# Kernel tuning notes

Hardware: AMD Instinct MI355X
Metric: run time of the kernel (lower is better)

The kernel has to match this reference:

```python
import jax, jax.numpy as jnp
import numpy as np

T, D, H, E, K = 8192, 512, 1024, 16, 2  # tokens, d_model, d_hidden, num_expert, top_k


def setup_inputs() -> dict:
    key = jax.random.key(0)
    ks = jax.random.split(key, 4)
    return {
        "x": jax.random.normal(ks[0], (T, D), jnp.float32),
        "Wg": jax.random.normal(ks[1], (D, E), jnp.float32) * (D ** -0.5),
        "bg": jnp.zeros((E,), jnp.float32),
        "W1": jax.random.normal(ks[2], (E, D, H), jnp.float32) * (D ** -0.5),
        "b1": jnp.zeros((E, H), jnp.float32),
        "W2": jax.random.normal(ks[3], (E, H, D), jnp.float32) * (H ** -0.5),
        "b2": jnp.zeros((E, D), jnp.float32),
    }


def _moe(x, Wg, bg, W1, b1, W2, b2):
    # NaiveGate: linear -> top-k -> softmax over the k selected logits
    logits = x @ Wg + bg                              # [T, E]
    top_val, top_idx = jax.lax.top_k(logits, K)       # [T, K]
    score = jax.nn.softmax(top_val, axis=-1)          # [T, K]
    # Dispatch + per-expert MLP + combine. Mathematically identical to the
    # scatter/grouped-GEMM/gather: for each expert, the per-token combine
    # weight is the gate score if the token routed there, else 0.
    out = jnp.zeros_like(x)
    for e in range(E):  # fixed small loop over structurally distinct experts
        h = jax.nn.gelu(x @ W1[e] + b1[e], approximate=False)  # [T, H]
        y = h @ W2[e] + b2[e]                                   # [T, D]
        w_e = jnp.sum(jnp.where(top_idx == e, score, 0.0), axis=-1)  # [T]
        out = out + w_e[:, None] * y
    return out


def reference(x, Wg, bg, W1, b1, W2, b2):
    return _moe(x, Wg, bg, W1, b1, W2, b2)
```

## Files before the change

kernel.cpp:

```cpp
#include <hip/hip_runtime.h>
#include <hip/hip_bf16.h>
#include <math.h>

#define TT 8192
#define DD 512
#define HH 1024
#define EE 16
#define NSLOT 18432
#define MAXTILES 144
#define BM 128
#define RETRYCAP 1024

typedef __attribute__((ext_vector_type(8))) short bf16x8;
typedef __attribute__((ext_vector_type(8))) unsigned short u16x8;
typedef __attribute__((ext_vector_type(4))) float f32x4;

__device__ __forceinline__ unsigned short f2bf(float f) {
  union { float f; unsigned u; } v; v.f = f;
  unsigned r = v.u + 0x7fffu + ((v.u >> 16) & 1u);
  return (unsigned short)(r >> 16);
}

__device__ __forceinline__ float bf2f(unsigned short u) {
  union { unsigned u; float f; } v; v.u = ((unsigned)u) << 16;
  return v.f;
}

__device__ __forceinline__ void gload16(const void* g, void* l) {
  __builtin_amdgcn_global_load_lds(
      (const __attribute__((address_space(1))) unsigned int*)g,
      (__attribute__((address_space(3))) unsigned int*)l, 16, 0, 0);
}

__device__ __forceinline__ float gelu_f(float v) {
  float s = fabsf(v) * 0.70710678118654752f;
  float t = 1.0f / (1.0f + 0.3275911f * s);
  float poly = t * (0.254829592f +
              t * (-0.284496736f +
              t * (1.421413741f +
              t * (-1.453152027f +
              t * 1.061405429f))));
  float erfa = 1.0f - poly * __expf(-s * s);
  float erfv = (v >= 0.f) ? erfa : -erfa;
  return 0.5f * v * (1.0f + erfv);
}

__device__ __forceinline__ int tile_decode(const int* __restrict__ counts,
                                           int mt, int* e_out, int* row0_out) {
  int off = 0, rem = mt;
#pragma unroll
  for (int q = 0; q < EE; q++) {
    int tl = (counts[q] + BM - 1) / BM;
    if (rem < tl) { *e_out = q; *row0_out = off + rem * BM; return 1; }
    rem -= tl;
    off += tl * BM;
  }
  return 0;
}

__global__ __launch_bounds__(256) void prep_kernel(
    const float* __restrict__ W1, const float* __restrict__ W2,
    unsigned short* __restrict__ w1t, unsigned short* __restrict__ w2t,
    const float* __restrict__ x, const float* __restrict__ Wg,
    const float* __restrict__ bg, unsigned short* __restrict__ xb,
    int* __restrict__ gate_e, float* __restrict__ gate_w,
    int* __restrict__ counts, int* __restrict__ nretry,
    int* __restrict__ retry) {
  __shared__ union { unsigned short t[64][68]; int cnt[EE]; } sm;
  int bid = blockIdx.x;
  int tid = threadIdx.x;
  if (bid < 128) {
    int lane = tid & 63;
    int wave = tid >> 6;
    int tok0 = bid * 64 + wave * 16;
    if (tid < EE) sm.cnt[tid] = 0;
    __syncthreads();
    int e = lane & 15;
    int kb = (lane >> 4) * 8;
    bf16x8 bfrag[16];
#pragma unroll
    for (int ks = 0; ks < 16; ks++) {
      int kbase = ks * 32 + kb;
#pragma unroll
      for (int j = 0; j < 8; j++)
        bfrag[ks][j] = (short)f2bf(Wg[(kbase + j) * EE + e]);
    }
    float bge = bg[e];
    f32x4 acc = {0.f, 0.f, 0.f, 0.f};
    const float* xrow = x + (size_t)(tok0 + (lane & 15)) * DD + kb;
    unsigned short* xbrow = xb + (size_t)(tok0 + (lane & 15)) * DD + kb;
#pragma unroll 4
    for (int ks = 0; ks < 16; ks++) {
      int k0 = ks * 32;
      float4 v0 = *(const float4*)(xrow + k0);
      float4 v1 = *(const float4*)(xrow + k0 + 4);
      u16x8 w0;
      w0[0] = f2bf(v0.x); w0[1] = f2bf(v0.y); w0[2] = f2bf(v0.z); w0[3] = f2bf(v0.w);
      w0[4] = f2bf(v1.x); w0[5] = f2bf(v1.y); w0[6] = f2bf(v1.z); w0[7] = f2bf(v1.w);
      *(u16x8*)(xbrow + k0) = w0;
      union { u16x8 u; bf16x8 b; } cv; cv.u = w0;
      acc = __builtin_amdgcn_mfma_f32_16x16x32_bf16(cv.b, bfrag[ks], acc, 0, 0, 0);
    }
#pragma unroll
    for (int r = 0; r < 4; r++) {
      float lf = acc[r] + bge;
      float v1 = -1e30f, v2 = -1e30f, v3 = -1e30f;
      int i1 = 0, i2 = 0;
#pragma unroll
      for (int q = 0; q < EE; q++) {
        float v = __shfl(lf, (lane & 48) | q);
        if (v > v1) { v3 = v2; v2 = v1; i2 = i1; v1 = v; i1 = q; }
        else if (v > v2) { v3 = v2; v2 = v; i2 = q; }
        else if (v > v3) { v3 = v; }
      }
      if ((lane & 15) == 0) {
        int t2 = tok0 + ((lane >> 4) << 2) + r;
        float p = expf(v2 - v1);
        float s = 1.0f / (1.0f + p);
        gate_e[t2 * 2] = i1;
        gate_e[t2 * 2 + 1] = i2;
        gate_w[t2 * 2] = s;
        gate_w[t2 * 2 + 1] = p * s;
        atomicAdd(&sm.cnt[i1], 1);
        atomicAdd(&sm.cnt[i2], 1);
        if (v2 - v3 < 0.02f) {
          int pos = atomicAdd(nretry, 1);
          if (pos < RETRYCAP) retry[pos] = t2;
        }
      }
    }
    __syncthreads();
    if (tid < EE) atomicAdd(&counts[tid], sm.cnt[tid]);
    return;
  }
  const float* src;
  unsigned short* dst;
  int R, C, c0, r0;
  int b = bid - 128;
  if (b < 2048) {
    int cx = b & 15, ry = (b >> 4) & 7, mat = b >> 7;
    src = W1 + (size_t)mat * DD * HH; dst = w1t + (size_t)mat * DD * HH;
    R = DD; C = HH; c0 = cx * 64; r0 = ry * 64;
  } else {
    b -= 2048;
    int cx = b & 7, ry = (b >> 3) & 15, mat = b >> 7;
    src = W2 + (size_t)mat * DD * HH; dst = w2t + (size_t)mat * DD * HH;
    R = HH; C = DD; c0 = cx * 64; r0 = ry * 64;
  }
#pragma unroll
  for (int p = 0; p < 4; p++) {
    int r = tid >> 2;
    int c4 = (tid & 3) + p * 4;
    float4 v = *(const float4*)(src + (size_t)(r0 + r) * C + c0 + c4 * 4);
    sm.t[c4 * 4 + 0][r] = f2bf(v.x);
    sm.t[c4 * 4 + 1][r] = f2bf(v.y);
    sm.t[c4 * 4 + 2][r] = f2bf(v.z);
    sm.t[c4 * 4 + 3][r] = f2bf(v.w);
  }
  __syncthreads();
#pragma unroll
  for (int p = 0; p < 4; p++) {
    int oc = (tid >> 4) + p * 16;
    int ch = tid & 15;
    ushort4 v = *(ushort4*)(&sm.t[oc][ch * 4]);
    *(ushort4*)(dst + (size_t)(c0 + oc) * R + r0 + ch * 4) = v;
  }
}

__global__ __launch_bounds__(256) void gatefix_kernel(
    const float* __restrict__ x, const float* __restrict__ Wg,
    const float* __restrict__ bg, const int* __restrict__ nretry,
    const int* __restrict__ retry, int* __restrict__ gate_e,
    float* __restrict__ gate_w, int* __restrict__ counts) {
  __shared__ float lg[16][17];
  __shared__ int toks[16];
  int tid = threadIdx.x;
  int sl = tid >> 4, e = tid & 15;
  int s = blockIdx.x * 16 + sl;
  int n = *nretry; if (n > RETRYCAP) n = RETRYCAP;
  int active = (s < n);
  int tok = 0;
  if (active) tok = retry[s];
  if (active) {
    const float* xr = x + (size_t)tok * DD;
    double a0 = 0.0, a1 = 0.0, a2 = 0.0, a3 = 0.0;
    for (int i = 0; i < DD / 4; i++) {
      a0 += (double)xr[i * 4 + 0] * (double)Wg[(i * 4 + 0) * EE + e];
      a1 += (double)xr[i * 4 + 1] * (double)Wg[(i * 4 + 1) * EE + e];
      a2 += (double)xr[i * 4 + 2] * (double)Wg[(i * 4 + 2) * EE + e];
      a3 += (double)xr[i * 4 + 3] * (double)Wg[(i * 4 + 3) * EE + e];
    }
    double acc = (a0 + a1) + (a2 + a3);
    lg[sl][e] = (float)(acc + (double)bg[e]);
    toks[sl] = tok;
  }
  __syncthreads();
  if (active && e == 0) {
    float v1 = -1e30f, v2 = -1e30f;
    int i1 = 0, i2 = 0;
#pragma unroll
    for (int q = 0; q < EE; q++) {
      float v = lg[sl][q];
      if (v > v1) { v2 = v1; i2 = i1; v1 = v; i1 = q; }
      else if (v > v2) { v2 = v; i2 = q; }
    }
    int t2 = toks[sl];
    int o1 = gate_e[t2 * 2], o2 = gate_e[t2 * 2 + 1];
    float p = expf(v2 - v1);
    float sc = 1.0f / (1.0f + p);
    gate_e[t2 * 2] = i1;
    gate_e[t2 * 2 + 1] = i2;
    gate_w[t2 * 2] = sc;
    gate_w[t2 * 2 + 1] = p * sc;
    if (o1 != i1 || o2 != i2) {
      atomicSub(&counts[o1], 1);
      atomicSub(&counts[o2], 1);
      atomicAdd(&counts[i1], 1);
      atomicAdd(&counts[i2], 1);
    }
  }
}

__global__ __launch_bounds__(256) void scatter_kernel(
    const int* __restrict__ gate_e, const float* __restrict__ gate_w,
    const int* __restrict__ counts, int* __restrict__ fill,
    int* __restrict__ slot_token, float* __restrict__ slot_w,
    int* __restrict__ slot_of) {
  __shared__ int lcnt[EE];
  __shared__ int lbase[EE];
  __shared__ int offs_s[EE];
  int tid = threadIdx.x;
  int t = blockIdx.x * 256 + tid;
  if (tid < EE) lcnt[tid] = 0;
  if (tid == 0) {
    int off = 0;
    for (int q = 0; q < EE; q++) {
      offs_s[q] = off;
      off += ((counts[q] + BM - 1) / BM) * BM;
    }
  }
  __syncthreads();
  if (blockIdx.x == 0) {
#pragma unroll
    for (int q = 0; q < EE; q++) {
      int cnt = counts[q];
      int lim = ((cnt + BM - 1) / BM) * BM;
      for (int p = cnt + tid; p < lim; p += 256)
        slot_token[offs_s[q] + p] = -1;
    }
  }
  int e0 = gate_e[t * 2], e1 = gate_e[t * 2 + 1];
  int p0 = atomicAdd(&lcnt[e0], 1);
  int p1 = atomicAdd(&lcnt[e1], 1);
  __syncthreads();
  if (tid < EE) lbase[tid] = atomicAdd(&fill[tid], lcnt[tid]);
  __syncthreads();
  int s0 = offs_s[e0] + lbase[e0] + p0;
  int s1 = offs_s[e1] + lbase[e1] + p1;
  slot_token[s0] = t;
  slot_w[s0] = gate_w[t * 2];
  slot_of[t * 2] = s0;
  slot_token[s1] = t;
  slot_w[s1] = gate_w[t * 2 + 1];
  slot_of[t * 2 + 1] = s1;
}

__global__ __launch_bounds__(256) void gemm1_kernel(
    const unsigned short* __restrict__ xb, const unsigned short* __restrict__ w1t,
    const float* __restrict__ b1, const int* __restrict__ slot_token,
    const int* __restrict__ counts, unsigned short* __restrict__ hb) {
  int e, row0;
  if (!tile_decode(counts, blockIdx.y, &e, &row0)) return;
  int n0 = blockIdx.x * 128;
  __shared__ unsigned short As[3][128][32];
  __shared__ unsigned short Bs[3][128][32];
  int tid = threadIdx.x;
  int lane = tid & 63;
  int wave = tid >> 6;
  int wm = wave >> 1, wn = wave & 1;
  int ra = tid >> 2, c = tid & 3;
  int tok_a = slot_token[row0 + ra]; if (tok_a < 0) tok_a = 0;
  int tok_b = slot_token[row0 + ra + 64]; if (tok_b < 0) tok_b = 0;
  const unsigned short* wbase = w1t + ((size_t)e * HH * DD);
  const unsigned short* gA0 = xb + (size_t)tok_a * DD + c * 8;
  const unsigned short* gA1 = xb + (size_t)tok_b * DD + c * 8;
  const unsigned short* gB0 = wbase + (size_t)(n0 + ra) * DD + c * 8;
  const unsigned short* gB1 = wbase + (size_t)(n0 + ra + 64) * DD + c * 8;
  f32x4 acc[4][4];
#pragma unroll
  for (int m = 0; m < 4; m++)
#pragma unroll
    for (int n = 0; n < 4; n++) {
      f32x4 z = {0.f, 0.f, 0.f, 0.f};
      acc[m][n] = z;
    }
  const int NK = DD / 32;
#pragma unroll
  for (int p = 0; p < 2; p++) {
    int kj = p * 32;
    gload16(gA0 + kj, &As[p][ra][c * 8]);
    gload16(gA1 + kj, &As[p][ra + 64][c * 8]);
    gload16(gB0 + kj, &Bs[p][ra][c * 8]);
    gload16(gB1 + kj, &Bs[p][ra + 64][c * 8]);
  }
  for (int kk = 0; kk < NK; kk++) {
    int cur = kk % 3;
    if (kk + 2 < NK) {
      int k2 = (kk + 2) * 32;
      int nx = (kk + 2) % 3;
      gload16(gA0 + k2, &As[nx][ra][c * 8]);
      gload16(gA1 + k2, &As[nx][ra + 64][c * 8]);
      gload16(gB0 + k2, &Bs[nx][ra][c * 8]);
      gload16(gB1 + k2, &Bs[nx][ra + 64][c * 8]);
      asm volatile("s_waitcnt vmcnt(8)" ::: "memory");
    } else if (kk + 1 < NK) {
      asm volatile("s_waitcnt vmcnt(4)" ::: "memory");
    } else {
      asm volatile("s_waitcnt vmcnt(0)" ::: "memory");
    }
    __builtin_amdgcn_s_barrier();
    bf16x8 a[4], b[4];
#pragma unroll
    for (int m = 0; m < 4; m++)
      a[m] = *(const bf16x8*)(&As[cur][wm * 64 + m * 16 + (lane & 15)][(lane >> 4) * 8]);
#pragma unroll
    for (int n = 0; n < 4; n++)
      b[n] = *(const bf16x8*)(&Bs[cur][wn * 64 + n * 16 + (lane & 15)][(lane >> 4) * 8]);
#pragma unroll
    for (int m = 0; m < 4; m++)
#pragma unroll
      for (int n = 0; n < 4; n++)
        acc[m][n] = __builtin_amdgcn_mfma_f32_16x16x32_bf16(a[m], b[n], acc[m][n], 0, 0, 0);
    asm volatile("" ::: "memory");
    __builtin_amdgcn_s_barrier();
  }
  const float* b1e = b1 + (size_t)e * HH;
#pragma unroll
  for (int m = 0; m < 4; m++) {
#pragma unroll
    for (int r = 0; r < 4; r++) {
      int slot = row0 + wm * 64 + m * 16 + ((lane >> 4) << 2) + r;
      unsigned short* hrow = hb + (size_t)slot * HH;
#pragma unroll
      for (int n = 0; n < 4; n++) {
        int hc = n0 + wn * 64 + n * 16 + (lane & 15);
        float v = acc[m][n][r] + b1e[hc];
        hrow[hc] = f2bf(gelu_f(v));
      }
    }
  }
}

template <int USE_Y>
__global__ __launch_bounds__(256) void gemm2_kernel(
    const unsigned short* __restrict__ hb, const unsigned short* __restrict__ w2t,
    const float* __restrict__ b2, const int* __restrict__ slot_token,
    const float* __restrict__ slot_w, const int* __restrict__ counts,
    unsigned short* __restrict__ yw, float* __restrict__ out) {
  int e, row0;
  if (!tile_decode(counts, blockIdx.y, &e, &row0)) return;
  int n0 = blockIdx.x * 128;
  __shared__ unsigned short As[3][128][32];
  __shared__ unsigned short Bs[3][128][32];
  int tid = threadIdx.x;
  int lane = tid & 63;
  int wave = tid >> 6;
  int wm = wave >> 1, wn = wave & 1;
  int ra = tid >> 2, c = tid & 3;
  const unsigned short* wbase = w2t + ((size_t)e * DD * HH);
  const unsigned short* gA0 = hb + (size_t)(row0 + ra) * HH + c * 8;
  const unsigned short* gA1 = hb + (size_t)(row0 + ra + 64) * HH + c * 8;
  const unsigned short* gB0 = wbase + (size_t)(n0 + ra) * HH + c * 8;
  const unsigned short* gB1 = wbase + (size_t)(n0 + ra + 64) * HH + c * 8;
  f32x4 acc[4][4];
#pragma unroll
  for (int m = 0; m < 4; m++)
#pragma unroll
    for (int n = 0; n < 4; n++) {
      f32x4 z = {0.f, 0.f, 0.f, 0.f};
      acc[m][n] = z;
    }
  const int NK = HH / 32;
#pragma unroll
  for (int p = 0; p < 2; p++) {
    int kj = p * 32;
    gload16(gA0 + kj, &As[p][ra][c * 8]);
    gload16(gA1 + kj, &As[p][ra + 64][c * 8]);
    gload16(gB0 + kj, &Bs[p][ra][c * 8]);
    gload16(gB1 + kj, &Bs[p][ra + 64][c * 8]);
  }
  for (int kk = 0; kk < NK; kk++) {
    int cur = kk % 3;
    if (kk + 2 < NK) {
      int k2 = (kk + 2) * 32;
      int nx = (kk + 2) % 3;
      gload16(gA0 + k2, &As[nx][ra][c * 8]);
      gload16(gA1 + k2, &As[nx][ra + 64][c * 8]);
      gload16(gB0 + k2, &Bs[nx][ra][c * 8]);
      gload16(gB1 + k2, &Bs[nx][ra + 64][c * 8]);
      asm volatile("s_waitcnt vmcnt(8)" ::: "memory");
    } else if (kk + 1 < NK) {
      asm volatile("s_waitcnt vmcnt(4)" ::: "memory");
    } else {
      asm volatile("s_waitcnt vmcnt(0)" ::: "memory");
    }
    __builtin_amdgcn_s_barrier();
    bf16x8 a[4], b[4];
#pragma unroll
    for (int m = 0; m < 4; m++)
      a[m] = *(const bf16x8*)(&As[cur][wm * 64 + m * 16 + (lane & 15)][(lane >> 4) * 8]);
#pragma unroll
    for (int n = 0; n < 4; n++)
      b[n] = *(const bf16x8*)(&Bs[cur][wn * 64 + n * 16 + (lane & 15)][(lane >> 4) * 8]);
#pragma unroll
    for (int m = 0; m < 4; m++)
#pragma unroll
      for (int n = 0; n < 4; n++)
        acc[m][n] = __builtin_amdgcn_mfma_f32_16x16x32_bf16(a[m], b[n], acc[m][n], 0, 0, 0);
    asm volatile("" ::: "memory");
    __builtin_amdgcn_s_barrier();
  }
  const float* b2e = b2 + (size_t)e * DD;
#pragma unroll
  for (int m = 0; m < 4; m++) {
#pragma unroll
    for (int r = 0; r < 4; r++) {
      int slot = row0 + wm * 64 + m * 16 + ((lane >> 4) << 2) + r;
      if (USE_Y) {
        float w = slot_w[slot];
        unsigned short* yrow = yw + (size_t)slot * DD;
#pragma unroll
        for (int n = 0; n < 4; n++) {
          int dc = n0 + wn * 64 + n * 16 + (lane & 15);
          yrow[dc] = f2bf(w * (acc[m][n][r] + b2e[dc]));
        }
      } else {
        int tok = slot_token[slot];
        if (tok >= 0) {
          float w = slot_w[slot];
          float* orow = out + (size_t)tok * DD;
#pragma unroll
          for (int n = 0; n < 4; n++) {
            int dc = n0 + wn * 64 + n * 16 + (lane & 15);
            float v = acc[m][n][r] + b2e[dc];
            atomicAdd(&orow[dc], w * v);
          }
        }
      }
    }
  }
}

__global__ __launch_bounds__(256) void combine_kernel(
    const unsigned short* __restrict__ yw, const int* __restrict__ slot_of,
    float* __restrict__ out) {
  int gid = blockIdx.x * 256 + threadIdx.x;
  int t = gid >> 6;
  int d0 = (gid & 63) * 8;
  int s1 = slot_of[t * 2], s2 = slot_of[t * 2 + 1];
  const ushort4* p1 = (const ushort4*)(yw + (size_t)s1 * DD + d0);
  const ushort4* p2 = (const ushort4*)(yw + (size_t)s2 * DD + d0);
  ushort4 a0 = p1[0], a1 = p1[1];
  ushort4 b0 = p2[0], b1 = p2[1];
  float4 o0, o1;
  o0.x = bf2f(a0.x) + bf2f(b0.x);
  o0.y = bf2f(a0.y) + bf2f(b0.y);
  o0.z = bf2f(a0.z) + bf2f(b0.z);
  o0.w = bf2f(a0.w) + bf2f(b0.w);
  o1.x = bf2f(a1.x) + bf2f(b1.x);
  o1.y = bf2f(a1.y) + bf2f(b1.y);
  o1.z = bf2f(a1.z) + bf2f(b1.z);
  o1.w = bf2f(a1.w) + bf2f(b1.w);
  float* orow = out + (size_t)t * DD + d0;
  ((float4*)orow)[0] = o0;
  ((float4*)orow)[1] = o1;
}

extern "C" void kernel_launch(void* const* d_in, const int* in_sizes, int n_in,
                              void* d_out, int out_size, void* d_ws, size_t ws_size,
                              hipStream_t stream) {
  const float* x  = (const float*)d_in[0];
  const float* Wg = (const float*)d_in[1];
  const float* bg = (const float*)d_in[2];
  const float* W1 = (const float*)d_in[3];
  const float* b1 = (const float*)d_in[4];
  const float* W2 = (const float*)d_in[5];
  const float* b2 = (const float*)d_in[6];
  float* out = (float*)d_out;

  uint8_t* w = (uint8_t*)d_ws;
  size_t o = 0;
  unsigned short* xb  = (unsigned short*)(w + o); o += (size_t)TT * DD * 2;
  unsigned short* w1t = (unsigned short*)(w + o); o += (size_t)EE * DD * HH * 2;
  unsigned short* w2t = (unsigned short*)(w + o); o += (size_t)EE * DD * HH * 2;
  unsigned short* hb  = (unsigned short*)(w + o); o += (size_t)NSLOT * HH * 2;
  int*   slot_token = (int*)(w + o);   o += (size_t)NSLOT * 4;
  float* slot_w     = (float*)(w + o); o += (size_t)NSLOT * 4;
  int*   slot_of    = (int*)(w + o);   o += (size_t)TT * 2 * 4;
  int*   gate_e     = (int*)(w + o);   o += (size_t)TT * 2 * 4;
  float* gate_w     = (float*)(w + o); o += (size_t)TT * 2 * 4;
  int*   counts     = (int*)(w + o);   o += 64;
  int*   nretry     = (int*)(w + o);   o += 64;
  int*   fill       = (int*)(w + o);   o += 64;
  int*   retry      = (int*)(w + o);   o += RETRYCAP * 4;
  unsigned short* yw = (unsigned short*)(w + o);
  size_t need_y = o + (size_t)NSLOT * DD * 2;
  int use_y = (ws_size >= need_y);

  hipMemsetAsync(counts, 0, 192, stream);
  if (!use_y) {
    hipMemsetAsync(slot_token, 0xFF, (size_t)NSLOT * 4, stream);
    hipMemsetAsync(d_out, 0, (size_t)TT * DD * 4, stream);
  }

  prep_kernel<<<128 + 4096, 256, 0, stream>>>(
      W1, W2, w1t, w2t, x, Wg, bg, xb, gate_e, gate_w, counts, nretry, retry);
  gatefix_kernel<<<RETRYCAP / 16, 256, 0, stream>>>(x, Wg, bg, nretry, retry,
                                                    gate_e, gate_w, counts);
  scatter_kernel<<<TT / 256, 256, 0, stream>>>(gate_e, gate_w, counts, fill,
                                               slot_token, slot_w, slot_of);
  {
    dim3 g(HH / 128, MAXTILES);
    gemm1_kernel<<<g, 256, 0, stream>>>(xb, w1t, b1, slot_token, counts, hb);
  }
  {
    dim3 g(DD / 128, MAXTILES);
    if (use_y)
      gemm2_kernel<1><<<g, 256, 0, stream>>>(hb, w2t, b2, slot_token, slot_w,
                                             counts, yw, out);
    else
      gemm2_kernel<0><<<g, 256, 0, stream>>>(hb, w2t, b2, slot_token, slot_w,
                                             counts, yw, out);
  }
  if (use_y) {
    combine_kernel<<<TT * (DD / 8) / 256, 256, 0, stream>>>(yw, slot_of, out);
  }
}
```

Measured before the change: 167.9 us.

## Widen GEMM tiles to 128x256 with 512 threads and double buffering

Both expert GEMMs now use 8 waves per block and a 128x256 output tile, halving the grid's N dimension. The shared-memory pipeline drops from triple to double buffering with one K-step of prefetch. Wider tiles let each A tile be reused across twice as many columns, cutting redundant global loads of gathered token rows. The costs are a shallower prefetch that may expose more memory latency, and fewer blocks in flight (grids of 4x144 and 2x144 on a 256-CU part), which risks poor load balance.

```diff
diff --git a/kernel.cpp b/kernel.cpp
--- a/kernel.cpp
+++ b/kernel.cpp
@@ -265,27 +265,25 @@
   slot_of[t * 2 + 1] = s1;
 }
 
-__global__ __launch_bounds__(256) void gemm1_kernel(
+__global__ __launch_bounds__(512) void gemm1_kernel(
     const unsigned short* __restrict__ xb, const unsigned short* __restrict__ w1t,
     const float* __restrict__ b1, const int* __restrict__ slot_token,
     const int* __restrict__ counts, unsigned short* __restrict__ hb) {
   int e, row0;
   if (!tile_decode(counts, blockIdx.y, &e, &row0)) return;
-  int n0 = blockIdx.x * 128;
-  __shared__ unsigned short As[3][128][32];
-  __shared__ unsigned short Bs[3][128][32];
+  int n0 = blockIdx.x * 256;
+  __shared__ unsigned short As[2][128][32];
+  __shared__ unsigned short Bs[2][256][32];
   int tid = threadIdx.x;
   int lane = tid & 63;
   int wave = tid >> 6;
-  int wm = wave >> 1, wn = wave & 1;
+  int wm = wave >> 2, wn = wave & 3;
   int ra = tid >> 2, c = tid & 3;
   int tok_a = slot_token[row0 + ra]; if (tok_a < 0) tok_a = 0;
-  int tok_b = slot_token[row0 + ra + 64]; if (tok_b < 0) tok_b = 0;
   const unsigned short* wbase = w1t + ((size_t)e * HH * DD);
-  const unsigned short* gA0 = xb + (size_t)tok_a * DD + c * 8;
-  const unsigned short* gA1 = xb + (size_t)tok_b * DD + c * 8;
+  const unsigned short* gA  = xb + (size_t)tok_a * DD + c * 8;
   const unsigned short* gB0 = wbase + (size_t)(n0 + ra) * DD + c * 8;
-  const unsigned short* gB1 = wbase + (size_t)(n0 + ra + 64) * DD + c * 8;
+  const unsigned short* gB1 = wbase + (size_t)(n0 + ra + 128) * DD + c * 8;
   f32x4 acc[4][4];
 #pragma unroll
   for (int m = 0; m < 4; m++)
@@ -295,26 +293,18 @@
       acc[m][n] = z;
     }
   const int NK = DD / 32;
-#pragma unroll
-  for (int p = 0; p < 2; p++) {
-    int kj = p * 32;
-    gload16(gA0 + kj, &As[p][ra][c * 8]);
-    gload16(gA1 + kj, &As[p][ra + 64][c * 8]);
-    gload16(gB0 + kj, &Bs[p][ra][c * 8]);
-    gload16(gB1 + kj, &Bs[p][ra + 64][c * 8]);
-  }
+  gload16(gA, &As[0][ra][c * 8]);
+  gload16(gB0, &Bs[0][ra][c * 8]);
+  gload16(gB1, &Bs[0][ra + 128][c * 8]);
   for (int kk = 0; kk < NK; kk++) {
-    int cur = kk % 3;
-    if (kk + 2 < NK) {
-      int k2 = (kk + 2) * 32;
-      int nx = (kk + 2) % 3;
-      gload16(gA0 + k2, &As[nx][ra][c * 8]);
-      gload16(gA1 + k2, &As[nx][ra + 64][c * 8]);
-      gload16(gB0 + k2, &Bs[nx][ra][c * 8]);
-      gload16(gB1 + k2, &Bs[nx][ra + 64][c * 8]);
-      asm volatile("s_waitcnt vmcnt(8)" ::: "memory");
-    } else if (kk + 1 < NK) {
-      asm volatile("s_waitcnt vmcnt(4)" ::: "memory");
+    int cur = kk & 1;
+    if (kk + 1 < NK) {
+      int k1 = (kk + 1) * 32;
+      int nx = cur ^ 1;
+      gload16(gA + k1, &As[nx][ra][c * 8]);
+      gload16(gB0 + k1, &Bs[nx][ra][c * 8]);
+      gload16(gB1 + k1, &Bs[nx][ra + 128][c * 8]);
+      asm volatile("s_waitcnt vmcnt(3)" ::: "memory");
     } else {
       asm volatile("s_waitcnt vmcnt(0)" ::: "memory");
     }
@@ -352,26 +342,25 @@
 }
 
 template <int USE_Y>
-__global__ __launch_bounds__(256) void gemm2_kernel(
+__global__ __launch_bounds__(512) void gemm2_kernel(
     const unsigned short* __restrict__ hb, const unsigned short* __restrict__ w2t,
     const float* __restrict__ b2, const int* __restrict__ slot_token,
     const float* __restrict__ slot_w, const int* __restrict__ counts,
     unsigned short* __restrict__ yw, float* __restrict__ out) {
   int e, row0;
   if (!tile_decode(counts, blockIdx.y, &e, &row0)) return;
-  int n0 = blockIdx.x * 128;
-  __shared__ unsigned short As[3][128][32];
-  __shared__ unsigned short Bs[3][128][32];
+  int n0 = blockIdx.x * 256;
+  __shared__ unsigned short As[2][128][32];
+  __shared__ unsigned short Bs[2][256][32];
   int tid = threadIdx.x;
   int lane = tid & 63;
   int wave = tid >> 6;
-  int wm = wave >> 1, wn = wave & 1;
+  int wm = wave >> 2, wn = wave & 3;
   int ra = tid >> 2, c = tid & 3;
   const unsigned short* wbase = w2t + ((size_t)e * DD * HH);
-  const unsigned short* gA0 = hb + (size_t)(row0 + ra) * HH + c * 8;
-  const unsigned short* gA1 = hb + (size_t)(row0 + ra + 64) * HH + c * 8;
+  const unsigned short* gA  = hb + (size_t)(row0 + ra) * HH + c * 8;
   const unsigned short* gB0 = wbase + (size_t)(n0 + ra) * HH + c * 8;
-  const unsigned short* gB1 = wbase + (size_t)(n0 + ra + 64) * HH + c * 8;
+  const unsigned short* gB1 = wbase + (size_t)(n0 + ra + 128) * HH + c * 8;
   f32x4 acc[4][4];
 #pragma unroll
   for (int m = 0; m < 4; m++)
@@ -381,26 +370,18 @@
       acc[m][n] = z;
     }
   const int NK = HH / 32;
-#pragma unroll
-  for (int p = 0; p < 2; p++) {
-    int kj = p * 32;
-    gload16(gA0 + kj, &As[p][ra][c * 8]);
-    gload16(gA1 + kj, &As[p][ra + 64][c * 8]);
-    gload16(gB0 + kj, &Bs[p][ra][c * 8]);
-    gload16(gB1 + kj, &Bs[p][ra + 64][c * 8]);
-  }
+  gload16(gA, &As[0][ra][c * 8]);
+  gload16(gB0, &Bs[0][ra][c * 8]);
+  gload16(gB1, &Bs[0][ra + 128][c * 8]);
   for (int kk = 0; kk < NK; kk++) {
-    int cur = kk % 3;
-    if (kk + 2 < NK) {
-      int k2 = (kk + 2) * 32;
-      int nx = (kk + 2) % 3;
-      gload16(gA0 + k2, &As[nx][ra][c * 8]);
-      gload16(gA1 + k2, &As[nx][ra + 64][c * 8]);
-      gload16(gB0 + k2, &Bs[nx][ra][c * 8]);
-      gload16(gB1 + k2, &Bs[nx][ra + 64][c * 8]);
-      asm volatile("s_waitcnt vmcnt(8)" ::: "memory");
-    } else if (kk + 1 < NK) {
-      asm volatile("s_waitcnt vmcnt(4)" ::: "memory");
+    int cur = kk & 1;
+    if (kk + 1 < NK) {
+      int k1 = (kk + 1) * 32;
+      int nx = cur ^ 1;
+      gload16(gA + k1, &As[nx][ra][c * 8]);
+      gload16(gB0 + k1, &Bs[nx][ra][c * 8]);
+      gload16(gB1 + k1, &Bs[nx][ra + 128][c * 8]);
+      asm volatile("s_waitcnt vmcnt(3)" ::: "memory");
     } else {
       asm volatile("s_waitcnt vmcnt(0)" ::: "memory");
     }
@@ -520,16 +501,16 @@
   scatter_kernel<<<TT / 256, 256, 0, stream>>>(gate_e, gate_w, counts, fill,
                                                slot_token, slot_w, slot_of);
   {
-    dim3 g(HH / 128, MAXTILES);
-    gemm1_kernel<<<g, 256, 0, stream>>>(xb, w1t, b1, slot_token, counts, hb);
+    dim3 g(HH / 256, MAXTILES);
+    gemm1_kernel<<<g, 512, 0, stream>>>(xb, w1t, b1, slot_token, counts, hb);
   }
   {
-    dim3 g(DD / 128, MAXTILES);
+    dim3 g(DD / 256, MAXTILES);
     if (use_y)
-      gemm2_kernel<1><<<g, 256, 0, stream>>>(hb, w2t, b2, slot_token, slot_w,
+      gemm2_kernel<1><<<g, 512, 0, stream>>>(hb, w2t, b2, slot_token, slot_w,
                                              counts, yw, out);
     else
-      gemm2_kernel<0><<<g, 256, 0, stream>>>(hb, w2t, b2, slot_token, slot_w,
+      gemm2_kernel<0><<<g, 512, 0, stream>>>(hb, w2t, b2, slot_token, slot_w,
                                              counts, yw, out);
   }
   if (use_y) {
```

Result: faster. 160.8 us (-4.2%).
